# Optimization experiments

Hardware: AMD Instinct MI355X
Metric: run time of the kernel (lower is better)

## Reference

```python
import jax, jax.numpy as jnp
import numpy as np

C = 512
GROUPS = 32
EPS = 1e-5


def group_norm(x, gamma, beta):
    # x: (B, C, H, W)
    B, Ch, H, W = x.shape
    xg = x.reshape(B, GROUPS, Ch // GROUPS, H, W)
    mu = xg.mean(axis=(2, 3, 4), keepdims=True)
    var = xg.var(axis=(2, 3, 4), keepdims=True)
    xn = ((xg - mu) * jax.lax.rsqrt(var + EPS)).reshape(B, Ch, H, W)
    return xn * gamma[None, :, None, None] + beta[None, :, None, None]


def conv1x1(x, w, b):
    # 1x1 conv == per-pixel matmul; x: (B,C,H,W), w: (Cout,Cin), b: (Cout,)
    return jnp.einsum('bchw,oc->bohw', x, w) + b[None, :, None, None]


def setup_inputs() -> dict:
    key = jax.random.key(0)
    ks = jax.random.split(key, 12)
    B, H, W = 4, 64, 64
    s = 1.0 / np.sqrt(C)
    inp = {
        'x': jax.random.normal(ks[0], (B, C, H, W), dtype=jnp.float32),
        'gn_w': jnp.ones((C,), dtype=jnp.float32),
        'gn_b': jnp.zeros((C,), dtype=jnp.float32),
        'wq': jax.random.uniform(ks[1], (C, C), jnp.float32, -s, s),
        'bq': jax.random.uniform(ks[2], (C,), jnp.float32, -s, s),
        'wk': jax.random.uniform(ks[3], (C, C), jnp.float32, -s, s),
        'bk': jax.random.uniform(ks[4], (C,), jnp.float32, -s, s),
        'wv': jax.random.uniform(ks[5], (C, C), jnp.float32, -s, s),
        'bv': jax.random.uniform(ks[6], (C,), jnp.float32, -s, s),
        'wo': jax.random.uniform(ks[7], (C, C), jnp.float32, -s, s),
        'bo': jax.random.uniform(ks[8], (C,), jnp.float32, -s, s),
    }
    return inp


def reference(x, gn_w, gn_b, wq, bq, wk, bk, wv, bv, wo, bo):
    B, Ch, H, W = x.shape
    h = group_norm(x, gn_w, gn_b)
    q = conv1x1(h, wq, bq).reshape(B, Ch, H * W)  # (B,C,HW)
    k = conv1x1(h, wk, bk).reshape(B, Ch, H * W)
    v = conv1x1(h, wv, bv).reshape(B, Ch, H * W)
    scale = 1.0 / jnp.sqrt(jnp.float32(Ch))
    # scores: (B, HW_q, HW_k)
    w = jnp.einsum('bcq,bck->bqk', q, k) * scale
    w = jax.nn.softmax(w, axis=-1)
    o = jnp.einsum('bqk,bck->bcq', w, v).reshape(B, Ch, H, W)
    o = conv1x1(o, wo, bo)
    return x + o
```

## Files before the change

### kernel.cpp

```cpp
#include <hip/hip_runtime.h>


typedef _Float16 f16;
typedef _Float16 f16x8 __attribute__((ext_vector_type(8)));
typedef _Float16 f16x4 __attribute__((ext_vector_type(4)));
typedef float f32x4 __attribute__((ext_vector_type(4)));

__device__ __forceinline__ void load_lds16(const void* g, void* l) {
  __builtin_amdgcn_global_load_lds(
      (const __attribute__((address_space(1))) unsigned int*)g,
      (__attribute__((address_space(3))) unsigned int*)l, 16, 0, 0);
}

__device__ __forceinline__ f32x4 mfma16(f16x8 a, f16x8 b, f32x4 c) {
  return __builtin_amdgcn_mfma_f32_16x16x32_f16(a, b, c, 0, 0, 0);
}

__global__ __launch_bounds__(256) void prep_weights(
    const float* __restrict__ wq, const float* __restrict__ bq,
    const float* __restrict__ wk, const float* __restrict__ bk,
    const float* __restrict__ wv, const float* __restrict__ wo,
    f16* __restrict__ Wqk, float* __restrict__ bqk,
    f16* __restrict__ Wv, f16* __restrict__ Wo) {
  const float s = 0.04419417382415922f;
  int i = blockIdx.x * 256 + threadIdx.x;
  if (i < 524288) {
    int row = i >> 9;
    Wqk[i] = (f16)((row < 512) ? wq[i] * s : wk[i - 262144]);
  } else if (i < 786432) {
    Wv[i - 524288] = (f16)wv[i - 524288];
  } else if (i < 1048576) {
    Wo[i - 786432] = (f16)wo[i - 786432];
  }
  if (i < 1024) bqk[i] = (i < 512) ? bq[i] * s : bk[i - 512];
}

__global__ __launch_bounds__(256) void gn_stats(const float* __restrict__ x,
                                                float2* __restrict__ stats) {
  long base = (long)blockIdx.x * 65536;
  int tid = threadIdx.x;
  float s = 0.f, ss = 0.f;
  for (int i = tid; i < 16384; i += 256) {
    float4 v = *(const float4*)&x[base + (long)i * 4];
    s += v.x + v.y + v.z + v.w;
    ss += v.x * v.x + v.y * v.y + v.z * v.z + v.w * v.w;
  }
#pragma unroll
  for (int o = 32; o; o >>= 1) {
    s += __shfl_xor(s, o);
    ss += __shfl_xor(ss, o);
  }
  __shared__ float rs[4], rss[4];
  if ((tid & 63) == 0) { rs[tid >> 6] = s; rss[tid >> 6] = ss; }
  __syncthreads();
  if (tid == 0) {
    s = rs[0] + rs[1] + rs[2] + rs[3];
    ss = rss[0] + rss[1] + rss[2] + rss[3];
    float mean = s * (1.f / 65536.f);
    float var = ss * (1.f / 65536.f) - mean * mean;
    stats[blockIdx.x] = make_float2(mean, rsqrtf(var + 1e-5f));
  }
}

__global__ __launch_bounds__(256) void gn_apply(
    const float* __restrict__ x, const float2* __restrict__ stats,
    const float* __restrict__ gnw, const float* __restrict__ gnb,
    f16* __restrict__ h_t) {
  int b = blockIdx.x >> 6;
  int p0 = (blockIdx.x & 63) * 64;
  int tid = threadIdx.x;
  __shared__ __align__(16) f16 lds[64 * 520];
  int c0 = tid >> 4;
  int p4 = tid & 15;
  for (int it = 0; it < 32; ++it) {
    int c = it * 16 + c0;
    float2 st = stats[b * 32 + (c >> 4)];
    float a = st.y * gnw[c];
    float sh = gnb[c] - st.x * a;
    float4 v = *(const float4*)&x[((long)(b * 512 + c)) * 4096 + p0 + p4 * 4];
    int pr = p4 * 4;
    lds[(pr + 0) * 520 + c] = (f16)(v.x * a + sh);
    lds[(pr + 1) * 520 + c] = (f16)(v.y * a + sh);
    lds[(pr + 2) * 520 + c] = (f16)(v.z * a + sh);
    lds[(pr + 3) * 520 + c] = (f16)(v.w * a + sh);
  }
  __syncthreads();
  for (int it = 0; it < 16; ++it) {
    int cid = it * 256 + tid;
    int prow = cid >> 6, c8 = (cid & 63) * 8;
    *(f16x8*)&h_t[((long)(b * 4096 + p0 + prow)) * 512 + c8] =
        *(const f16x8*)&lds[prow * 520 + c8];
  }
}

template <int MODE>
__global__ __launch_bounds__(256) void gemm_bt(
    const f16* __restrict__ A, int lda, long sAz,
    const f16* __restrict__ B, int ldb, long sBz,
    void* __restrict__ C, int ldc, long sCz,
    const float* __restrict__ bias,
    const float* __restrict__ resid, long sRz,
    int M, int N, int K) {
  __shared__ __align__(16) f16 tA[4096];
  __shared__ __align__(16) f16 tB[4096];
  const f16* Az = A + (long)blockIdx.z * sAz;
  const f16* Bz = B + (long)blockIdx.z * sBz;
  int tid = threadIdx.x, lane = tid & 63, wid = tid >> 6;
  long bm = (long)blockIdx.x * 128, bn = (long)blockIdx.y * 128;
  int srow = lane >> 2, scol = (lane & 3) * 8;
  int wrow = (wid >> 1) * 64, wcol = (wid & 1) * 64;
  int r = lane & 15, kb = (lane >> 4) * 8;

  const f16* gA0 = Az + (bm + wid * 32 + srow) * (long)lda + scol;
  const f16* gA1 = gA0 + 16 * (long)lda;
  const f16* gB0 = Bz + (bn + wid * 32 + srow) * (long)ldb + scol;
  const f16* gB1 = gB0 + 16 * (long)ldb;
  f16* lA0 = &tA[wid * 1024];
  f16* lA1 = &tA[wid * 1024 + 512];
  f16* lB0 = &tB[wid * 1024];
  f16* lB1 = &tB[wid * 1024 + 512];

  f32x4 acc[4][4];
#pragma unroll
  for (int i = 0; i < 4; ++i)
#pragma unroll
    for (int j = 0; j < 4; ++j) acc[i][j] = (f32x4){0.f, 0.f, 0.f, 0.f};

  for (int kt = 0; kt < K; kt += 32) {
    load_lds16(gA0 + kt, lA0);
    load_lds16(gA1 + kt, lA1);
    load_lds16(gB0 + kt, lB0);
    load_lds16(gB1 + kt, lB1);
    __syncthreads();
    f16x8 af[4], bfr[4];
#pragma unroll
    for (int mf = 0; mf < 4; ++mf)
      af[mf] = *(const f16x8*)&tA[(wrow + mf * 16 + r) * 32 + kb];
#pragma unroll
    for (int nf = 0; nf < 4; ++nf)
      bfr[nf] = *(const f16x8*)&tB[(wcol + nf * 16 + r) * 32 + kb];
#pragma unroll
    for (int mf = 0; mf < 4; ++mf)
#pragma unroll
      for (int nf = 0; nf < 4; ++nf)
        acc[mf][nf] = mfma16(af[mf], bfr[nf], acc[mf][nf]);
    __syncthreads();
  }

  long zC = (long)blockIdx.z * sCz;
  int r0 = (lane >> 4) * 4, cc = lane & 15;
#pragma unroll
  for (int mf = 0; mf < 4; ++mf) {
#pragma unroll
    for (int rr = 0; rr < 4; ++rr) {
      long R = bm + wrow + mf * 16 + r0 + rr;
      float badd = 0.f;
      if constexpr (MODE == 1 || MODE == 3) badd = bias[R];
#pragma unroll
      for (int nf = 0; nf < 4; ++nf) {
        long gc = bn + wcol + nf * 16 + cc;
        float v = acc[mf][nf][rr];
        if constexpr (MODE == 0) v += bias[gc];
        if constexpr (MODE == 1) v += badd;
        if constexpr (MODE == 3)
          v += badd + resid[(long)blockIdx.z * sRz + R * (long)ldc + gc];
        long idx = zC + R * (long)ldc + gc;
        if constexpr (MODE == 3)
          ((float*)C)[idx] = v;
        else
          ((f16*)C)[idx] = (f16)v;
      }
    }
  }
}

__global__ __launch_bounds__(512, 2) void attn_fused3(
    const f16* __restrict__ qk_t, const f16* __restrict__ v_ws,
    f16* __restrict__ o_t) {
  __shared__ __align__(16) f16 KL[2][32][512];
  __shared__ __align__(16) f16 PL[64][32];
  __shared__ float LS[2][64];

  const int tid = threadIdx.x;
  const int lane = tid & 63, w = tid >> 6;
  const int lq = lane & 15, lg = lane >> 4;
  const int qt = w & 3, kh = w >> 2;
  const int bid = blockIdx.x;
  const int z = (bid >> 1) & 3;
  const int qblk = ((bid >> 3) << 1) | (bid & 1);
  const long bm = (long)qblk * 64;
  const f16* Qb = qk_t + (long)z * 4096 * 1024;
  const f16* Kb = Qb + 512;
  const f16* Vb = v_ws + (long)z * 4096;

  f16x8 qf[16];
#pragma unroll
  for (int s = 0; s < 16; ++s)
    qf[s] = *(const f16x8*)&Qb[(bm + qt * 16 + lq) * 1024 + s * 32 + lg * 8];

  f32x4 acc[4][4];
#pragma unroll
  for (int i = 0; i < 4; ++i)
#pragma unroll
    for (int j = 0; j < 4; ++j) acc[i][j] = (f32x4){0.f, 0.f, 0.f, 0.f};
  float rs = 0.f;

  auto stageK = [&](int kt, int b) {
#pragma unroll
    for (int i = 0; i < 4; ++i) {
      int row = w * 4 + i;
      load_lds16(
          &Kb[((long)(kt * 32 + row)) * 1024 + ((lane * 8) ^ ((row & 7) * 8))],
          &KL[b][row][0]);
    }
  };

  stageK(0, 0);
  __syncthreads();

  for (int kt = 0; kt < 128; ++kt) {
    const int cur = kt & 1;
    f16x8 vf[4];
#pragma unroll
    for (int dt = 0; dt < 4; ++dt)
      vf[dt] = *(const f16x8*)
          &Vb[(long)(w * 64 + dt * 16 + lq) * 16384 + kt * 32 + lg * 8];
    if (kt + 1 < 128) stageK(kt + 1, cur ^ 1);

    const int arow = kh * 16 + lq;
    const f16* klrow = &KL[cur][arow][0];
    const int sw = (arow & 7) * 8;
    f32x4 saA = (f32x4){0.f, 0.f, 0.f, 0.f};
    f32x4 saB = (f32x4){0.f, 0.f, 0.f, 0.f};
#pragma unroll
    for (int s = 0; s < 16; s += 2) {
      f16x8 k0 = *(const f16x8*)&klrow[(s * 32 + lg * 8) ^ sw];
      f16x8 k1 = *(const f16x8*)&klrow[((s + 1) * 32 + lg * 8) ^ sw];
      saA = mfma16(k0, qf[s], saA);
      saB = mfma16(k1, qf[s + 1], saB);
    }
    f32x4 sa = saA + saB;

    f16x4 pa;
    float ps = 0.f;
#pragma unroll
    for (int rr = 0; rr < 4; ++rr) {
      float e = __expf(fminf(sa[rr], 11.f));
      ps += e;
      pa[rr] = (f16)e;
    }
    rs += ps;
    *(f16x4*)&PL[qt * 16 + lq][kh * 16 + lg * 4] = pa;

    asm volatile("s_waitcnt lgkmcnt(0)" ::: "memory");
    __builtin_amdgcn_sched_barrier(0);
    __builtin_amdgcn_s_barrier();
    __builtin_amdgcn_sched_barrier(0);

    f16x8 pfr[4];
#pragma unroll
    for (int q4 = 0; q4 < 4; ++q4)
      pfr[q4] = *(const f16x8*)&PL[q4 * 16 + lq][lg * 8];
#pragma unroll
    for (int q4 = 0; q4 < 4; ++q4)
#pragma unroll
      for (int dt = 0; dt < 4; ++dt)
        acc[q4][dt] = mfma16(pfr[q4], vf[dt], acc[q4][dt]);

    __syncthreads();
  }

  rs += __shfl_xor(rs, 16);
  rs += __shfl_xor(rs, 32);
  if (lane < 16) LS[kh][qt * 16 + lane] = rs;
  __syncthreads();

  f16* orow = o_t + ((long)z * 4096 + bm) * 512 + w * 64;
#pragma unroll
  for (int q4 = 0; q4 < 4; ++q4) {
    float li[4];
#pragma unroll
    for (int rr = 0; rr < 4; ++rr) {
      int q = q4 * 16 + lg * 4 + rr;
      li[rr] = 1.f / (LS[0][q] + LS[1][q]);
    }
#pragma unroll
    for (int dt = 0; dt < 4; ++dt)
#pragma unroll
      for (int rr = 0; rr < 4; ++rr)
        orow[(long)(q4 * 16 + lg * 4 + rr) * 512 + dt * 16 + lq] =
            (f16)(acc[q4][dt][rr] * li[rr]);
  }
}

extern "C" void kernel_launch(void* const* d_in, const int* in_sizes, int n_in,
                              void* d_out, int out_size, void* d_ws,
                              size_t ws_size, hipStream_t stream) {
  (void)in_sizes; (void)n_in; (void)out_size; (void)ws_size;
  const float* x   = (const float*)d_in[0];
  const float* gnw = (const float*)d_in[1];
  const float* gnb = (const float*)d_in[2];
  const float* wq  = (const float*)d_in[3];
  const float* bq  = (const float*)d_in[4];
  const float* wk  = (const float*)d_in[5];
  const float* bk  = (const float*)d_in[6];
  const float* wv  = (const float*)d_in[7];
  const float* bv  = (const float*)d_in[8];
  const float* wo  = (const float*)d_in[9];
  const float* bo  = (const float*)d_in[10];
  float* out = (float*)d_out;

  char* p = (char*)d_ws;
  auto alloc = [&](size_t bytes) {
    char* r = p;
    p += (bytes + 255) & ~(size_t)255;
    return r;
  };
  f16* Wqk    = (f16*)alloc(1024 * 512 * 2);
  float* bqk  = (float*)alloc(1024 * 4);
  f16* Wv     = (f16*)alloc(512 * 512 * 2);
  f16* Wo     = (f16*)alloc(512 * 512 * 2);
  float2* st  = (float2*)alloc(128 * 8);
  f16* h_t    = (f16*)alloc(16384L * 512 * 2);
  f16* qk_t   = (f16*)alloc(16384L * 1024 * 2);
  f16* v_ws   = (f16*)alloc(512L * 16384 * 2);
  f16* o_t    = (f16*)alloc(16384L * 512 * 2);

  prep_weights<<<4096, 256, 0, stream>>>(wq, bq, wk, bk, wv, wo, Wqk, bqk, Wv,
                                         Wo);
  gn_stats<<<128, 256, 0, stream>>>(x, st);
  gn_apply<<<256, 256, 0, stream>>>(x, st, gnw, gnb, h_t);

  gemm_bt<0><<<dim3(128, 8, 1), 256, 0, stream>>>(
      h_t, 512, 0, Wqk, 512, 0, qk_t, 1024, 0, bqk, nullptr, 0,
      16384, 1024, 512);
  gemm_bt<1><<<dim3(4, 128, 1), 256, 0, stream>>>(
      Wv, 512, 0, h_t, 512, 0, v_ws, 16384, 0, bv, nullptr, 0,
      512, 16384, 512);

  attn_fused3<<<256, 512, 0, stream>>>(qk_t, v_ws, o_t);

  gemm_bt<3><<<dim3(4, 32, 4), 256, 0, stream>>>(
      Wo, 512, 0, o_t, 512, 4096L * 512, out, 4096, 512L * 4096,
      bo, x, 512L * 4096, 512, 4096, 512);
}
```

Baseline: 437.5 us.

## Split attention over key halves with partial outputs and a merge kernel

Splits the attention kernel's key range in two (split-K), launching twice as many blocks that each write unnormalized partial outputs and row sums, then adds a merge kernel that sums the halves and normalizes. The K tile buffer becomes single-buffered, with the next stage issued after the barrier, to cut LDS use so that four blocks per CU can be requested. This targets low occupancy and too few blocks on a large GPU. In exchange it adds extra fp16 partial-output traffic, an extra launch, less overlap of K loads, and possible register pressure at four waves per SIMD. Skipping the running max is safe only because the exponent is clamped, as in the prior version.

```diff
diff --git a/kernel.cpp b/kernel.cpp
--- a/kernel.cpp
+++ b/kernel.cpp
@@ -174,10 +174,10 @@
   }
 }
 
-__global__ __launch_bounds__(512, 2) void attn_fused3(
+__global__ __launch_bounds__(512, 4) void attn_fused4(
     const f16* __restrict__ qk_t, const f16* __restrict__ v_ws,
-    f16* __restrict__ o_t) {
-  __shared__ __align__(16) f16 KL[2][32][512];
+    f16* __restrict__ o_part, float* __restrict__ lpart) {
+  __shared__ __align__(16) f16 KL[32][512];
   __shared__ __align__(16) f16 PL[64][32];
   __shared__ float LS[2][64];
 
@@ -186,9 +186,11 @@
   const int lq = lane & 15, lg = lane >> 4;
   const int qt = w & 3, kh = w >> 2;
   const int bid = blockIdx.x;
+  const int khalf = bid & 1;
   const int z = (bid >> 1) & 3;
-  const int qblk = ((bid >> 3) << 1) | (bid & 1);
+  const int qblk = bid >> 3;
   const long bm = (long)qblk * 64;
+  const int kbase = khalf * 2048;
   const f16* Qb = qk_t + (long)z * 4096 * 1024;
   const f16* Kb = Qb + 512;
   const f16* Vb = v_ws + (long)z * 4096;
@@ -205,30 +207,28 @@
     for (int j = 0; j < 4; ++j) acc[i][j] = (f32x4){0.f, 0.f, 0.f, 0.f};
   float rs = 0.f;
 
-  auto stageK = [&](int kt, int b) {
+  auto stageK = [&](int kt) {
 #pragma unroll
     for (int i = 0; i < 4; ++i) {
       int row = w * 4 + i;
-      load_lds16(
-          &Kb[((long)(kt * 32 + row)) * 1024 + ((lane * 8) ^ ((row & 7) * 8))],
-          &KL[b][row][0]);
+      load_lds16(&Kb[((long)(kbase + kt * 32 + row)) * 1024 +
+                     ((lane * 8) ^ ((row & 7) * 8))],
+                 &KL[row][0]);
     }
   };
 
-  stageK(0, 0);
+  stageK(0);
   __syncthreads();
 
-  for (int kt = 0; kt < 128; ++kt) {
-    const int cur = kt & 1;
+  for (int kt = 0; kt < 64; ++kt) {
     f16x8 vf[4];
 #pragma unroll
     for (int dt = 0; dt < 4; ++dt)
-      vf[dt] = *(const f16x8*)
-          &Vb[(long)(w * 64 + dt * 16 + lq) * 16384 + kt * 32 + lg * 8];
-    if (kt + 1 < 128) stageK(kt + 1, cur ^ 1);
+      vf[dt] = *(const f16x8*)&Vb[(long)(w * 64 + dt * 16 + lq) * 16384 +
+                                  kbase + kt * 32 + lg * 8];
 
     const int arow = kh * 16 + lq;
-    const f16* klrow = &KL[cur][arow][0];
+    const f16* klrow = &KL[arow][0];
     const int sw = (arow & 7) * 8;
     f32x4 saA = (f32x4){0.f, 0.f, 0.f, 0.f};
     f32x4 saB = (f32x4){0.f, 0.f, 0.f, 0.f};
@@ -257,6 +257,8 @@
     __builtin_amdgcn_s_barrier();
     __builtin_amdgcn_sched_barrier(0);
 
+    if (kt + 1 < 64) stageK(kt + 1);
+
     f16x8 pfr[4];
 #pragma unroll
     for (int q4 = 0; q4 < 4; ++q4)
@@ -274,23 +276,38 @@
   rs += __shfl_xor(rs, 32);
   if (lane < 16) LS[kh][qt * 16 + lane] = rs;
   __syncthreads();
-
-  f16* orow = o_t + ((long)z * 4096 + bm) * 512 + w * 64;
-#pragma unroll
-  for (int q4 = 0; q4 < 4; ++q4) {
-    float li[4];
-#pragma unroll
-    for (int rr = 0; rr < 4; ++rr) {
-      int q = q4 * 16 + lg * 4 + rr;
-      li[rr] = 1.f / (LS[0][q] + LS[1][q]);
-    }
+  if (tid < 64)
+    lpart[((long)(khalf * 4 + z)) * 4096 + bm + tid] =
+        LS[0][tid] + LS[1][tid];
+
+  f16* orow = o_part + (((long)(khalf * 4 + z)) * 4096 + bm) * 512 + w * 64;
+#pragma unroll
+  for (int q4 = 0; q4 < 4; ++q4)
 #pragma unroll
     for (int dt = 0; dt < 4; ++dt)
 #pragma unroll
       for (int rr = 0; rr < 4; ++rr)
         orow[(long)(q4 * 16 + lg * 4 + rr) * 512 + dt * 16 + lq] =
-            (f16)(acc[q4][dt][rr] * li[rr]);
-  }
+            (f16)acc[q4][dt][rr];
+}
+
+__global__ __launch_bounds__(256) void attn_merge(
+    const f16* __restrict__ o_part, const float* __restrict__ lpart,
+    f16* __restrict__ o_t) {
+  long gid = (long)blockIdx.x * 256 + threadIdx.x;
+  long row = gid >> 6;
+  int z = (int)(row >> 12);
+  long zp = row;
+  int c8 = (int)(gid & 63) * 8;
+  float linv = 1.f / (lpart[(long)z * 4096 + (zp & 4095)] +
+                      lpart[(long)(4 + z) * 4096 + (zp & 4095)]);
+  f16x8 a = *(const f16x8*)&o_part[(((long)z) * 4096 + (zp & 4095)) * 512 + c8];
+  f16x8 b = *(const f16x8*)
+      &o_part[(((long)(4 + z)) * 4096 + (zp & 4095)) * 512 + c8];
+  f16x8 o;
+#pragma unroll
+  for (int j = 0; j < 8; ++j) o[j] = (f16)(((float)a[j] + (float)b[j]) * linv);
+  *(f16x8*)&o_t[zp * 512 + c8] = o;
 }
 
 extern "C" void kernel_launch(void* const* d_in, const int* in_sizes, int n_in,
@@ -325,6 +342,8 @@
   f16* qk_t   = (f16*)alloc(16384L * 1024 * 2);
   f16* v_ws   = (f16*)alloc(512L * 16384 * 2);
   f16* o_t    = (f16*)alloc(16384L * 512 * 2);
+  f16* o_part = (f16*)alloc(2 * 16384L * 512 * 2);
+  float* lprt = (float*)alloc(2 * 16384L * 4);
 
   prep_weights<<<4096, 256, 0, stream>>>(wq, bq, wk, bk, wv, wo, Wqk, bqk, Wv,
                                          Wo);
@@ -338,7 +357,8 @@
       Wv, 512, 0, h_t, 512, 0, v_ws, 16384, 0, bv, nullptr, 0,
       512, 16384, 512);
 
-  attn_fused3<<<256, 512, 0, stream>>>(qk_t, v_ws, o_t);
+  attn_fused4<<<512, 512, 0, stream>>>(qk_t, v_ws, o_part, lprt);
+  attn_merge<<<4096, 256, 0, stream>>>(o_part, lprt, o_t);
 
   gemm_bt<3><<<dim3(4, 32, 4), 256, 0, stream>>>(
       Wo, 512, 0, o_t, 512, 4096L * 512, out, 4096, 512L * 4096,
```

Measured after the change: 957.5 us. 119% more time.
